# Performance work log

Measured on AMD Instinct MI355X. Metric: run time of the kernel, lower is better.

The kernel has to match this reference:

```python
import jax, jax.numpy as jnp
import numpy as np

B, N, D2H, U = 16, 1024, 1024, 512  # batch of sentences, tokens, 2*lstm_dims, hidden_units


def setup_inputs() -> dict:
    key = jax.random.key(0)
    ks = jax.random.split(key, 7)
    s = 1.0 / np.sqrt(D2H)
    return {
        "x": jax.random.normal(ks[0], (B, N, D2H), dtype=jnp.float32),
        "W_h": jax.random.normal(ks[1], (U, D2H), dtype=jnp.float32) * s,
        "b_h": jax.random.normal(ks[2], (U,), dtype=jnp.float32) * 0.01,
        "W_m": jax.random.normal(ks[3], (U, D2H), dtype=jnp.float32) * s,
        "b_m": jax.random.normal(ks[4], (U,), dtype=jnp.float32) * 0.01,
        "w_out": jax.random.normal(ks[5], (U,), dtype=jnp.float32) * (1.0 / np.sqrt(U)),
        "b_out": jax.random.normal(ks[6], (), dtype=jnp.float32) * 0.01,
    }


def reference(x, W_h, b_h, W_m, b_m, w_out, b_out):
    # headfov[i] = W_h @ x_i + b_h ; modfov[j] = W_m @ x_j + b_m
    H = jnp.einsum("bnd,ud->bnu", x, W_h) + b_h  # [B, N, U]
    M = jnp.einsum("bnd,ud->bnu", x, W_m) + b_m  # [B, N, U]
    # score[i,j] = w_out . (H_i + M_j) + b_out  (outLayer is linear, so it
    # distributes over the add; avoids materializing an [B,N,N,U] tensor)
    sH = jnp.einsum("bnu,u->bn", H, w_out)  # [B, N]
    sM = jnp.einsum("bnu,u->bn", M, w_out)  # [B, N]
    scores = sH[:, :, None] + sM[:, None, :] + b_out  # [B, N, N]
    return scores
```

## Files before the change

kernel.cpp:

```cpp
#include <hip/hip_runtime.h>

#define BB 16
#define NN 1024
#define DD 1024
#define UU 512

__global__ __launch_bounds__(256) void prep_kernel(
    const float* __restrict__ W_h, const float* __restrict__ W_m,
    const float* __restrict__ b_h, const float* __restrict__ b_m,
    const float* __restrict__ w_out, const float* __restrict__ b_out,
    float* __restrict__ v_h, float* __restrict__ v_m, float* __restrict__ Cc) {
    int t = threadIdx.x;
    int blk = blockIdx.x;
    if (blk < 256) {
        const float* W = (blk < 128) ? W_h : W_m;
        float* v = (blk < 128) ? v_h : v_m;
        int b = blk & 127;
        int d = (b & 3) * 256 + t;
        int u0 = (b >> 2) * 16;
        float acc = 0.f;
        #pragma unroll
        for (int k = 0; k < 16; ++k) {
            acc += W[(size_t)(u0 + k) * DD + d] * w_out[u0 + k];
        }
        atomicAdd(v + d, acc);
    } else {
        __shared__ float red[256];
        float acc = 0.f;
        for (int u = t; u < UU; u += 256) acc += (b_h[u] + b_m[u]) * w_out[u];
        red[t] = acc;
        __syncthreads();
        for (int s = 128; s > 0; s >>= 1) {
            if (t < s) red[t] += red[t + s];
            __syncthreads();
        }
        if (t == 0) *Cc = red[0] + b_out[0];
    }
}

__global__ __launch_bounds__(256) void row_dots_kernel(
    const float* __restrict__ x,
    const float* __restrict__ v_h, const float* __restrict__ v_m,
    const float* __restrict__ Cc,
    float* __restrict__ sH, float* __restrict__ sM) {
    __shared__ float4 lvh[DD / 4];
    __shared__ float4 lvm[DD / 4];
    int t = threadIdx.x;
    lvh[t] = ((const float4*)v_h)[t];
    lvm[t] = ((const float4*)v_m)[t];
    __syncthreads();

    int wave = t >> 6, lane = t & 63;
    int row0 = blockIdx.x * 16 + wave * 4;
    float C = *Cc;

    #pragma unroll
    for (int r = 0; r < 4; ++r) {
        int row = row0 + r;
        const float4* xr = (const float4*)(x + (size_t)row * DD);
        float ah = 0.f, am = 0.f;
        #pragma unroll
        for (int k = 0; k < 4; ++k) {
            int idx = lane + 64 * k;
            float4 xv = xr[idx];
            float4 hv = lvh[idx];
            float4 mv = lvm[idx];
            ah += xv.x * hv.x + xv.y * hv.y + xv.z * hv.z + xv.w * hv.w;
            am += xv.x * mv.x + xv.y * mv.y + xv.z * mv.z + xv.w * mv.w;
        }
        #pragma unroll
        for (int off = 32; off > 0; off >>= 1) {
            ah += __shfl_down(ah, off, 64);
            am += __shfl_down(am, off, 64);
        }
        if (lane == 0) {
            sH[row] = ah + C;
            sM[row] = am;
        }
    }
}

__global__ __launch_bounds__(256) void scores_kernel(
    const float* __restrict__ sH, const float* __restrict__ sM,
    float4* __restrict__ out) {
    int bi = blockIdx.x;
    int j4 = threadIdx.x;
    float h = sH[bi];
    const float4* mrow = (const float4*)(sM + (bi & ~(NN - 1)));
    float4 m = mrow[j4];
    float4 o;
    o.x = h + m.x;
    o.y = h + m.y;
    o.z = h + m.z;
    o.w = h + m.w;
    out[(size_t)bi * (NN / 4) + j4] = o;
}

extern "C" void kernel_launch(void* const* d_in, const int* in_sizes, int n_in,
                              void* d_out, int out_size, void* d_ws, size_t ws_size,
                              hipStream_t stream) {
    const float* x     = (const float*)d_in[0];
    const float* W_h   = (const float*)d_in[1];
    const float* b_h   = (const float*)d_in[2];
    const float* W_m   = (const float*)d_in[3];
    const float* b_m   = (const float*)d_in[4];
    const float* w_out = (const float*)d_in[5];
    const float* b_out = (const float*)d_in[6];
    float* out = (float*)d_out;

    float* ws  = (float*)d_ws;
    float* v_h = ws;
    float* v_m = ws + 1024;
    float* Cc  = ws + 2048;
    float* sH  = ws + 4096;
    float* sM  = ws + 4096 + 16384;

    (void)hipMemsetAsync(ws, 0, 2048 * sizeof(float), stream);

    prep_kernel<<<257, 256, 0, stream>>>(W_h, W_m, b_h, b_m, w_out, b_out, v_h, v_m, Cc);
    row_dots_kernel<<<BB * NN / 16, 256, 0, stream>>>(x, v_h, v_m, Cc, sH, sM);
    scores_kernel<<<BB * NN, 256, 0, stream>>>(sH, sM, (float4*)out);
}
```

Baseline: 129.6 us.

## Fuse prep, row-dot and scores kernels into one cooperative kernel with grid syncs

Merges the three kernels into a single cooperative launch of 512 blocks that uses grid-wide syncs between the weight-vector reduction, the per-row dot products and the output broadcast. Each block now handles 32 rows in both later phases and reuses one loaded sM vector across its 32 output rows. The aim is to remove two kernel launch gaps and the many tiny scores blocks. In exchange it adds two grid barriers and leaves fewer blocks streaming the 64 MB output write.

Measured after the change: 270.3 us. 2.09x slower.

```diff
diff --git a/kernel.cpp b/kernel.cpp
--- a/kernel.cpp
+++ b/kernel.cpp
@@ -1,17 +1,27 @@
 #include <hip/hip_runtime.h>
+#include <hip/hip_cooperative_groups.h>
+
+namespace cg = cooperative_groups;
 
 #define BB 16
 #define NN 1024
 #define DD 1024
 #define UU 512
+#define GRID 512
 
-__global__ __launch_bounds__(256) void prep_kernel(
-    const float* __restrict__ W_h, const float* __restrict__ W_m,
-    const float* __restrict__ b_h, const float* __restrict__ b_m,
+__global__ __launch_bounds__(256, 2) void fused_kernel(
+    const float* __restrict__ x,
+    const float* __restrict__ W_h, const float* __restrict__ b_h,
+    const float* __restrict__ W_m, const float* __restrict__ b_m,
     const float* __restrict__ w_out, const float* __restrict__ b_out,
-    float* __restrict__ v_h, float* __restrict__ v_m, float* __restrict__ Cc) {
+    float* __restrict__ v_h, float* __restrict__ v_m, float* __restrict__ Cc,
+    float* __restrict__ sH, float* __restrict__ sM,
+    float4* __restrict__ out) {
+    cg::grid_group grid = cg::this_grid();
+    __shared__ float4 lv[DD / 2];
     int t = threadIdx.x;
     int blk = blockIdx.x;
+
     if (blk < 256) {
         const float* W = (blk < 128) ? W_h : W_m;
         float* v = (blk < 128) ? v_h : v_m;
@@ -24,8 +34,8 @@
             acc += W[(size_t)(u0 + k) * DD + d] * w_out[u0 + k];
         }
         atomicAdd(v + d, acc);
-    } else {
-        __shared__ float red[256];
+    } else if (blk == 256) {
+        float* red = (float*)lv;
         float acc = 0.f;
         for (int u = t; u < UU; u += 256) acc += (b_h[u] + b_m[u]) * w_out[u];
         red[t] = acc;
@@ -36,64 +46,59 @@
         }
         if (t == 0) *Cc = red[0] + b_out[0];
     }
-}
 
-__global__ __launch_bounds__(256) void row_dots_kernel(
-    const float* __restrict__ x,
-    const float* __restrict__ v_h, const float* __restrict__ v_m,
-    const float* __restrict__ Cc,
-    float* __restrict__ sH, float* __restrict__ sM) {
-    __shared__ float4 lvh[DD / 4];
-    __shared__ float4 lvm[DD / 4];
-    int t = threadIdx.x;
-    lvh[t] = ((const float4*)v_h)[t];
-    lvm[t] = ((const float4*)v_m)[t];
+    grid.sync();
+
+    lv[t]       = ((const float4*)v_h)[t];
+    lv[256 + t] = ((const float4*)v_m)[t];
     __syncthreads();
-
+    float C = *Cc;
     int wave = t >> 6, lane = t & 63;
-    int row0 = blockIdx.x * 16 + wave * 4;
-    float C = *Cc;
-
-    #pragma unroll
-    for (int r = 0; r < 4; ++r) {
-        int row = row0 + r;
-        const float4* xr = (const float4*)(x + (size_t)row * DD);
-        float ah = 0.f, am = 0.f;
-        #pragma unroll
-        for (int k = 0; k < 4; ++k) {
-            int idx = lane + 64 * k;
-            float4 xv = xr[idx];
-            float4 hv = lvh[idx];
-            float4 mv = lvm[idx];
-            ah += xv.x * hv.x + xv.y * hv.y + xv.z * hv.z + xv.w * hv.w;
-            am += xv.x * mv.x + xv.y * mv.y + xv.z * mv.z + xv.w * mv.w;
-        }
-        #pragma unroll
-        for (int off = 32; off > 0; off >>= 1) {
-            ah += __shfl_down(ah, off, 64);
-            am += __shfl_down(am, off, 64);
-        }
-        if (lane == 0) {
-            sH[row] = ah + C;
-            sM[row] = am;
+    {
+        int rbase = blk * 32 + wave * 8;
+        #pragma unroll 2
+        for (int r = 0; r < 8; ++r) {
+            int row = rbase + r;
+            const float4* xr = (const float4*)(x + (size_t)row * DD);
+            float ah = 0.f, am = 0.f;
+            #pragma unroll
+            for (int k = 0; k < 4; ++k) {
+                int idx = lane + 64 * k;
+                float4 xv = xr[idx];
+                float4 hv = lv[idx];
+                float4 mv = lv[256 + idx];
+                ah += xv.x * hv.x + xv.y * hv.y + xv.z * hv.z + xv.w * hv.w;
+                am += xv.x * mv.x + xv.y * mv.y + xv.z * mv.z + xv.w * mv.w;
+            }
+            #pragma unroll
+            for (int off = 32; off > 0; off >>= 1) {
+                ah += __shfl_down(ah, off, 64);
+                am += __shfl_down(am, off, 64);
+            }
+            if (lane == 0) {
+                sH[row] = ah + C;
+                sM[row] = am;
+            }
         }
     }
-}
 
-__global__ __launch_bounds__(256) void scores_kernel(
-    const float* __restrict__ sH, const float* __restrict__ sM,
-    float4* __restrict__ out) {
-    int bi = blockIdx.x;
-    int j4 = threadIdx.x;
-    float h = sH[bi];
-    const float4* mrow = (const float4*)(sM + (bi & ~(NN - 1)));
-    float4 m = mrow[j4];
-    float4 o;
-    o.x = h + m.x;
-    o.y = h + m.y;
-    o.z = h + m.z;
-    o.w = h + m.w;
-    out[(size_t)bi * (NN / 4) + j4] = o;
+    grid.sync();
+
+    {
+        int bi0 = blk * 32;
+        const float4* mrow = (const float4*)(sM + (bi0 & ~(NN - 1)));
+        float4 m = mrow[t];
+        #pragma unroll 4
+        for (int s = 0; s < 32; ++s) {
+            float h = sH[bi0 + s];
+            float4 o;
+            o.x = h + m.x;
+            o.y = h + m.y;
+            o.z = h + m.z;
+            o.w = h + m.w;
+            out[(size_t)(bi0 + s) * (NN / 4) + t] = o;
+        }
+    }
 }
 
 extern "C" void kernel_launch(void* const* d_in, const int* in_sizes, int n_in,
@@ -106,7 +111,7 @@
     const float* b_m   = (const float*)d_in[4];
     const float* w_out = (const float*)d_in[5];
     const float* b_out = (const float*)d_in[6];
-    float* out = (float*)d_out;
+    float4* out = (float4*)d_out;
 
     float* ws  = (float*)d_ws;
     float* v_h = ws;
@@ -117,7 +122,8 @@
 
     (void)hipMemsetAsync(ws, 0, 2048 * sizeof(float), stream);
 
-    prep_kernel<<<257, 256, 0, stream>>>(W_h, W_m, b_h, b_m, w_out, b_out, v_h, v_m, Cc);
-    row_dots_kernel<<<BB * NN / 16, 256, 0, stream>>>(x, v_h, v_m, Cc, sH, sM);
-    scores_kernel<<<BB * NN, 256, 0, stream>>>(sH, sM, (float4*)out);
+    void* args[] = {&x, &W_h, &b_h, &W_m, &b_m, &w_out, &b_out,
+                    &v_h, &v_m, &Cc, &sH, &sM, &out};
+    (void)hipLaunchCooperativeKernel((void*)fused_kernel, dim3(GRID), dim3(256),
+                                     args, 0, stream);
 }
```
